# Optimization experiments

Hardware: AMD Instinct MI355X
Metric: run time of the kernel (lower is better)

## Reference

```python
import jax, jax.numpy as jnp
import numpy as np

K_NEIGHBORS = 16
NUM_PATCHES = 32
W_NORMAL = 1.0
W_SURFVAR = 1.0


def _knn_centered(points, k):
    """points: [B, N, 3] -> k nearest neighbors re-centered at each point, [B, N, k, 3].
    Distances are computed on stop_gradient(points) to match torch's .detach()."""
    pd = jax.lax.stop_gradient(points)
    # squared pairwise distances [B, N, N] (sqrt is monotone -> topk order identical)
    d2 = jnp.sum((pd[:, :, None, :] - pd[:, None, :, :]) ** 2, axis=-1)
    _, idx = jax.lax.top_k(-d2, k)  # smallest-k indices, [B, N, k]
    knn = jax.vmap(lambda pts, id_: pts[id_])(points, idx)  # [B, N, k, 3]
    return knn - points[:, :, None, :]


def _eig_props(knn):
    """knn: [B, N, k, 3] -> (normal [B,N,3] = eigvec of smallest eigval, eigvals [B,N,3] ascending)."""
    cov = jnp.einsum('bnki,bnkj->bnij', knn, knn)  # [B, N, 3, 3]
    w, v = jnp.linalg.eigh(cov)  # ascending eigenvalues, matches torch.symeig
    return v[..., :, 0], w


def setup_inputs() -> dict:
    key = jax.random.key(0)
    pointCloud = jax.random.normal(key, (4, 8192, 3), dtype=jnp.float32)
    return {"pointCloud": pointCloud}


def reference(pointCloud):
    B, N, _ = pointCloud.shape
    pp = N // NUM_PATCHES

    # global kNN / normals / surface variance
    knn_g = _knn_centered(pointCloud, K_NEIGHBORS)
    nrm_g, w_g = _eig_props(knn_g)

    # patchwise: each patch is an independent small point cloud -> fold patches into batch
    patch_pts = pointCloud.reshape(B * NUM_PATCHES, pp, 3)
    knn_p = _knn_centered(patch_pts, K_NEIGHBORS)
    nrm_p, w_p = _eig_props(knn_p)
    nrm_p = nrm_p.reshape(B, N, 3)

    # normal loss (abs variant, sign-ambiguity-free)
    loss_n = jnp.mean(jnp.linalg.norm(jnp.abs(nrm_p) - jnp.abs(nrm_g), axis=2)) * W_NORMAL

    # surface variance loss: lambda_min / sum(lambda)
    sv_g = w_g[..., 0] / jnp.sum(w_g, axis=-1)            # [B, N]
    sv_p = (w_p[..., 0] / jnp.sum(w_p, axis=-1)).reshape(B, N)
    loss_sv = jnp.mean((sv_p - sv_g) ** 2) * W_SURFVAR

    return jnp.stack([loss_n, loss_sv])  # [2] (original returns list of two [1] tensors)
```

## Files before the change

### kernel.cpp

```cpp
#include <hip/hip_runtime.h>
#include <math.h>

#define KNN 16
#define NPTS 8192
#define PTCH 256
#define NPATCH 32
#define NBATCH 4
#define NQ 32
#define SSTRIDE 130
#define LAMBDA_T 64.0f

#define NC 16
#define NCELLS (NC * NC * NC)
#define GMIN -4.2f
#define ICS 1.9047619f

__device__ __forceinline__ float lam_f(float r, float s)
{
    const float C     = 0.063493636f;
    const float SQ2PI = 2.5066283f;
    const float IS2   = 0.70710678f;
    float a = fabsf(r - s), b = r + s;
    float amr = a - r;
    float coefA = amr * amr + 2.f - s * s;
    float I = 2.f * __expf(-0.5f * b * b) - coefA * __expf(-0.5f * a * a)
            + r * SQ2PI * (erff(b * IS2) - erff(a * IS2));
    float M = C * (3.14159265f / r) * I;
    if (s > r) {
        float u = s - r;
        M += 12.566371f * C * (1.2533141f * erff(u * IS2) - u * __expf(-0.5f * u * u));
    }
    return (float)NPTS * M;
}

__device__ __forceinline__ void jrot(double& app, double& aqq, double& apq,
                                     double& arp, double& arq,
                                     double& vp0, double& vq0,
                                     double& vp1, double& vq1,
                                     double& vp2, double& vq2)
{
    double g = apq;
    if (g == 0.0) return;
    double theta = (aqq - app) / (2.0 * g);
    double at = fabs(theta);
    double t = (at > 1.0e154) ? (0.5 / theta)
                              : (copysign(1.0, theta) / (at + sqrt(theta * theta + 1.0)));
    double c = 1.0 / sqrt(t * t + 1.0);
    double s = t * c;
    double tau = s / (1.0 + c);
    app -= t * g;
    aqq += t * g;
    apq = 0.0;
    double rp = arp, rq = arq;
    arp = rp - s * (rq + tau * rp);
    arq = rq + s * (rp - tau * rq);
    double p0 = vp0, q0 = vq0;
    vp0 = p0 - s * (q0 + tau * p0); vq0 = q0 + s * (p0 - tau * q0);
    double p1 = vp1, q1 = vq1;
    vp1 = p1 - s * (q1 + tau * p1); vq1 = q1 + s * (p1 - tau * q1);
    double p2 = vp2, q2 = vq2;
    vp2 = p2 - s * (q2 + tau * p2); vq2 = q2 + s * (p2 - tau * q2);
}

__device__ __forceinline__ void eig3(double a00, double a11, double a22,
                                     double a01, double a02, double a12,
                                     double& nx, double& ny, double& nz,
                                     double& lmin, double& lsum)
{
    double v00 = 1, v01 = 0, v02 = 0;
    double v10 = 0, v11 = 1, v12 = 0;
    double v20 = 0, v21 = 0, v22 = 1;
    double scale = fabs(a00) + fabs(a11) + fabs(a22) + fabs(a01) + fabs(a02) + fabs(a12);
    if (scale > 0.0) {
        for (int sweep = 0; sweep < 6; ++sweep) {
            double off = fabs(a01) + fabs(a02) + fabs(a12);
            if (off <= scale * 1e-15) break;
            jrot(a00, a11, a01, a02, a12, v00, v01, v10, v11, v20, v21);
            jrot(a00, a22, a02, a01, a12, v00, v02, v10, v12, v20, v22);
            jrot(a11, a22, a12, a01, a02, v01, v02, v11, v12, v21, v22);
        }
    }
    lsum = a00 + a11 + a22;
    lmin = a00; nx = v00; ny = v10; nz = v20;
    if (a11 < lmin) { lmin = a11; nx = v01; ny = v11; nz = v21; }
    if (a22 < lmin) { lmin = a22; nx = v02; ny = v12; nz = v22; }
}

__device__ __forceinline__ unsigned mkkey(float d2, unsigned idx) {
    return (__float_as_uint(d2) & 0xFFFFE000u) | idx;
}

__device__ __forceinline__ void insert16(unsigned key, unsigned* L)
{
    L[KNN - 1] = key;
    #pragma unroll
    for (int m = KNN - 1; m >= 1; --m) {
        unsigned a = L[m - 1], b = L[m];
        L[m - 1] = min(a, b);
        L[m]     = max(a, b);
    }
}

__device__ __forceinline__ void merge4(unsigned* L, int lane)
{
    #pragma unroll
    for (int step = 1; step <= 2; step <<= 1) {
        unsigned tmp[KNN];
        #pragma unroll
        for (int m = 0; m < KNN; ++m) tmp[m] = __shfl(L[m], lane ^ step, 64);
        for (int m = 0; m < KNN; ++m) {
            if (tmp[m] >= L[KNN - 1]) break;
            insert16(tmp[m], L);
        }
    }
}

__device__ __forceinline__ float rfl(float x) {
    return __int_as_float(__builtin_amdgcn_readfirstlane(__float_as_int(x)));
}
__device__ __forceinline__ unsigned mbcnt64(unsigned long long m) {
    return __builtin_amdgcn_mbcnt_hi((unsigned)(m >> 32),
           __builtin_amdgcn_mbcnt_lo((unsigned)m, 0u));
}

__device__ __forceinline__ int cidx(float v) {
    int i = (int)floorf((v - GMIN) * ICS);
    return min(max(i, 0), NC - 1);
}
__device__ __forceinline__ int cellOf(float x, float y, float z) {
    return (cidx(z) * NC + cidx(y)) * NC + cidx(x);
}

#define BT 1024
__global__ void __launch_bounds__(1024)
build_kernel(const float* __restrict__ pts, float* __restrict__ out,
             unsigned* __restrict__ cellStart, float4* __restrict__ sorted)
{
    __shared__ unsigned hist[NCELLS];
    __shared__ unsigned part[BT];
    const int b = blockIdx.x;
    const int t = threadIdx.x;
    if (b == 0 && t == 0) { out[0] = 0.0f; out[1] = 0.0f; }
    for (int i = t; i < NCELLS; i += BT) hist[i] = 0u;
    __syncthreads();
    const float* base = pts + (size_t)b * (NPTS * 3);
    float px[8], py[8], pz[8];
    int pc[8];
    #pragma unroll
    for (int k = 0; k < 8; ++k) {
        int i = k * BT + t;
        px[k] = base[i * 3 + 0];
        py[k] = base[i * 3 + 1];
        pz[k] = base[i * 3 + 2];
        pc[k] = cellOf(px[k], py[k], pz[k]);
        atomicAdd(&hist[pc[k]], 1u);
    }
    __syncthreads();
    unsigned loc[4], s = 0;
    #pragma unroll
    for (int i = 0; i < 4; ++i) { loc[i] = s; s += hist[t * 4 + i]; }
    part[t] = s;
    __syncthreads();
    for (int o = 1; o < BT; o <<= 1) {
        unsigned u = (t >= o) ? part[t - o] : 0u;
        __syncthreads();
        part[t] += u;
        __syncthreads();
    }
    unsigned basex = part[t] - s;
    unsigned* csb = cellStart + b * (NCELLS + 1);
    #pragma unroll
    for (int i = 0; i < 4; ++i) {
        unsigned e = basex + loc[i];
        csb[t * 4 + i] = e;
        hist[t * 4 + i] = e;
    }
    if (t == BT - 1) csb[NCELLS] = basex + s;
    __syncthreads();
    float4* sb = sorted + (size_t)b * NPTS;
    #pragma unroll
    for (int k = 0; k < 8; ++k) {
        int i = k * BT + t;
        unsigned slot = atomicAdd(&hist[pc[k]], 1u);
        float4 v;
        v.x = px[k]; v.y = py[k]; v.z = pz[k]; v.w = __uint_as_float((unsigned)i);
        sb[slot] = v;
    }
}

__global__ void __launch_bounds__(256)
gate_kernel(const float* __restrict__ pts, float* __restrict__ g2buf)
{
    int q = blockIdx.x * 256 + threadIdx.x;
    int b = q >> 13, i = q & (NPTS - 1);
    const float* pp = pts + (size_t)b * (NPTS * 3) + (size_t)i * 3;
    float x = pp[0], y = pp[1], z = pp[2];
    float r = fmaxf(sqrtf(x * x + y * y + z * z), 0.01f);
    float lo = 0.f, hi = 12.f;
    #pragma unroll 1
    for (int it = 0; it < 16; ++it) {
        float mid = 0.5f * (lo + hi);
        if (lam_f(r, mid) < LAMBDA_T) lo = mid; else hi = mid;
    }
    g2buf[q] = hi * hi;
}

__global__ void __launch_bounds__(256)
filter_kernel(const float* __restrict__ pts, const float* __restrict__ g2buf,
              const unsigned* __restrict__ cellStart,
              const float4* __restrict__ sortedp,
              unsigned* __restrict__ survk, unsigned* __restrict__ cnts)
{
    const int lane = threadIdx.x & 63;
    const int wq = __builtin_amdgcn_readfirstlane(
        (int)((blockIdx.x * 256u + (unsigned)threadIdx.x) >> 6));
    const int b  = wq >> 13;
    const int qi = wq & (NPTS - 1);
    const float* base = pts + (size_t)b * (NPTS * 3);
    const unsigned* cs = cellStart + b * (NCELLS + 1);
    const float4* sp = sortedp + (size_t)b * NPTS;

    const float qx = base[qi * 3 + 0];
    const float qy = base[qi * 3 + 1];
    const float qz = base[qi * 3 + 2];
    const float g2 = g2buf[wq];
    const float g  = sqrtf(g2);

    int ixlo = cidx(qx - g), ixhi = cidx(qx + g);
    int iylo = cidx(qy - g), iyhi = cidx(qy + g);
    int izlo = cidx(qz - g), izhi = cidx(qz + g);
    int nx = ixhi - ixlo + 1;
    int ny = iyhi - iylo + 1;
    int nyz = ny * (izhi - izlo + 1);
    const int lR  = (nyz >= 8) ? 3 : (nyz >= 4) ? 2 : (nyz >= 2) ? 1 : 0;
    const int R   = 1 << lR;
    const int lsl = 6 - lR;
    const unsigned SL = 64u >> lR;
    const unsigned slot = (unsigned)lane & (SL - 1u);
    unsigned cnt = 0;
    unsigned sbase = (unsigned)wq * SSTRIDE;
    #pragma unroll 1
    for (int r0 = 0; r0 < nyz; r0 += 64) {
        int r = r0 + lane;
        unsigned pk = 0;
        if (r < nyz) {
            int iz = izlo + r / ny;
            int iy = iylo + (r - (r / ny) * ny);
            int cb = (iz * NC + iy) * NC + ixlo;
            unsigned sB = cs[cb];
            pk = sB | ((cs[cb + nx] - sB) << 14);
        }
        int rmax = min(nyz - r0, 64);
        int gcount = (rmax + R - 1) >> lR;
        #pragma unroll 1
        for (int gg = 0; gg < gcount; ++gg) {
            unsigned pkm = __shfl(pk, (gg << lR) + (lane >> lsl), 64);
            unsigned sBm = pkm & 0x3FFFu;
            unsigned lm  = pkm >> 14;
            #pragma unroll 1
            for (unsigned st = slot; ; st += SL) {
                bool in = st < lm;
                if (!__any(in ? 1 : 0)) break;
                float4 c = sp[min(sBm + st, (unsigned)(NPTS - 1))];
                float dx = qx - c.x, dy = qy - c.y, dz = qz - c.z;
                float d2 = dx * dx + dy * dy + dz * dz;
                bool pass = in && (d2 < g2);
                unsigned long long m = __ballot(pass);
                if (pass) {
                    unsigned sw = min(cnt + mbcnt64(m), (unsigned)(SSTRIDE - 1));
                    survk[sbase + sw] = mkkey(d2, __float_as_uint(c.w));
                }
                cnt += (unsigned)__popcll(m);
            }
        }
    }
    if (lane == 0) cnts[wq] = cnt;
}

__global__ void __launch_bounds__(256, 4)
select_kernel(const float* __restrict__ pts,
              const float* __restrict__ g2buf,
              const unsigned* __restrict__ survk_g,
              const unsigned* __restrict__ cnts_g,
              double* __restrict__ partials)
{
    __shared__ float4 pbuf4[PTCH];
    __shared__ unsigned survl[NQ * SSTRIDE];
    __shared__ unsigned cnts[NQ];
    __shared__ double xbuf[NQ * 4];
    __shared__ double rb[4];

    const int t = threadIdx.x;
    const int w = t >> 6;
    const int lane = t & 63;
    const int p = blockIdx.x;
    const int eighth = blockIdx.y;
    const int b = blockIdx.z;

    const float* base = pts + (size_t)b * (NPTS * 3);
    const int qbase = p * PTCH + eighth * NQ;
    const int qg0 = b * NPTS + qbase;

    {
        const float* src = base + p * (PTCH * 3);
        float* dst = (float*)pbuf4;
        #pragma unroll
        for (int s = 0; s < 3; ++s) {
            int f = t + s * 256;
            int j = f / 3;
            int c = f - 3 * j;
            dst[j * 4 + c] = src[f];
        }
    }
    {
        const unsigned* src = survk_g + (size_t)qg0 * SSTRIDE;
        #pragma unroll 1
        for (int i = t; i < NQ * SSTRIDE; i += 256) survl[i] = src[i];
        if (t < NQ) cnts[t] = cnts_g[qg0 + t];
    }
    __syncthreads();

    const int qq = lane >> 2;
    const int h = lane & 3;
    const int myq = (w & 1) * 16 + qq;
    float4 qv = pbuf4[eighth * NQ + myq];
    const float pqx = qv.x, pqy = qv.y, pqz = qv.z;

    double ngx = 0, ngy = 0, ngz = 0, svg = 0;

    if (w < 2) {
        unsigned gl[KNN];
        #pragma unroll
        for (int m = 0; m < KNN; ++m) gl[m] = 0xFFFFFFFFu;
        unsigned cnt = cnts[myq];
        bool valid = (cnt >= KNN) && (cnt <= SSTRIDE);
        if (valid) {
            unsigned share = (cnt + 3) >> 2;
            unsigned m0 = h * share;
            unsigned m1 = min(m0 + share, cnt);
            #pragma unroll 4
            for (unsigned m = m0; m < m1; ++m) {
                unsigned k = survl[myq * SSTRIDE + m];
                if (k < gl[KNN - 1]) insert16(k, gl);
            }
        }
        merge4(gl, lane);
        if (valid) {
            float g = g2buf[qg0 + myq];
            float upper = __uint_as_float((gl[KNN - 1] & 0xFFFFE000u) + 0x2000u);
            valid = (upper < g * 0.999f - 1e-5f);
        }
        if (__any((h == 0 && !valid) ? 1 : 0)) {
            if (h == 0 && !valid) {
                #pragma unroll
                for (int m = 0; m < KNN; ++m) gl[m] = 0xFFFFFFFFu;
                #pragma unroll 1
                for (int i = 0; i < NPTS; ++i) {
                    float cx = base[i * 3 + 0];
                    float cy = base[i * 3 + 1];
                    float cz = base[i * 3 + 2];
                    float dx = pqx - cx, dy = pqy - cy, dz = pqz - cz;
                    float d2 = dx * dx + dy * dy + dz * dz;
                    unsigned k = mkkey(d2, (unsigned)i);
                    if (k < gl[KNN - 1]) insert16(k, gl);
                }
            }
        }
        if (h == 0) {
            double c00 = 0, c11 = 0, c22 = 0, c01 = 0, c02 = 0, c12 = 0;
            const double qxd = pqx, qyd = pqy, qzd = pqz;
            #pragma unroll
            for (int m = 0; m < KNN; ++m) {
                int idx = (int)(gl[m] & 0x1FFFu);
                double dx = (double)base[idx * 3 + 0] - qxd;
                double dy = (double)base[idx * 3 + 1] - qyd;
                double dz = (double)base[idx * 3 + 2] - qzd;
                c00 += dx * dx; c11 += dy * dy; c22 += dz * dz;
                c01 += dx * dy; c02 += dx * dz; c12 += dy * dz;
            }
            double lmin, lsum;
            eig3(c00, c11, c22, c01, c02, c12, ngx, ngy, ngz, lmin, lsum);
            svg = lmin / lsum;
        }
    } else {
        unsigned pl[KNN];
        #pragma unroll
        for (int m = 0; m < KNN; ++m) pl[m] = 0xFFFFFFFFu;
        const int j0 = h * 64;
        #pragma unroll 4
        for (int j = j0; j < j0 + 64; ++j) {
            float4 c = pbuf4[j];
            float dx = pqx - c.x, dy = pqy - c.y, dz = pqz - c.z;
            float d2 = dx * dx + dy * dy + dz * dz;
            unsigned k = mkkey(d2, (unsigned)j);
            if (k < pl[KNN - 1]) insert16(k, pl);
        }
        merge4(pl, lane);
        if (h == 0) {
            double c00 = 0, c11 = 0, c22 = 0, c01 = 0, c02 = 0, c12 = 0;
            const double qxd = pqx, qyd = pqy, qzd = pqz;
            #pragma unroll
            for (int m = 0; m < KNN; ++m) {
                int idx = (int)(pl[m] & 0x1FFFu);
                float4 cpt = pbuf4[idx];
                double dx = (double)cpt.x - qxd;
                double dy = (double)cpt.y - qyd;
                double dz = (double)cpt.z - qzd;
                c00 += dx * dx; c11 += dy * dy; c22 += dz * dz;
                c01 += dx * dy; c02 += dx * dz; c12 += dy * dz;
            }
            double nx, ny, nz, lmin, lsum;
            eig3(c00, c11, c22, c01, c02, c12, nx, ny, nz, lmin, lsum);
            xbuf[myq * 4 + 0] = nx;
            xbuf[myq * 4 + 1] = ny;
            xbuf[myq * 4 + 2] = nz;
            xbuf[myq * 4 + 3] = lmin / lsum;
        }
    }
    __syncthreads();

    double ln = 0.0, lsv = 0.0;
    if (w < 2 && h == 0) {
        double npx = xbuf[myq * 4 + 0];
        double npy = xbuf[myq * 4 + 1];
        double npz = xbuf[myq * 4 + 2];
        double svp = xbuf[myq * 4 + 3];
        double dx = fabs(npx) - fabs(ngx);
        double dy = fabs(npy) - fabs(ngy);
        double dz = fabs(npz) - fabs(ngz);
        ln  = sqrt(dx * dx + dy * dy + dz * dz);
        double ds = svp - svg;
        lsv = ds * ds;
    }
    if (w < 2) {
        #pragma unroll
        for (int o = 32; o > 0; o >>= 1) {
            ln  += __shfl_down(ln, o);
            lsv += __shfl_down(lsv, o);
        }
        if (lane == 0) { rb[w * 2 + 0] = ln; rb[w * 2 + 1] = lsv; }
    }
    __syncthreads();
    if (t == 0) {
        const int bf = (b * 8 + eighth) * NPATCH + p;
        partials[bf * 2 + 0] = rb[0] + rb[2];
        partials[bf * 2 + 1] = rb[1] + rb[3];
    }
}

__global__ void __launch_bounds__(256)
reduce_kernel(const double* __restrict__ partials, float* __restrict__ out)
{
    __shared__ double sln[4], slv[4];
    const int t = threadIdx.x;
    double a = 0.0, c = 0.0;
    #pragma unroll
    for (int k = 0; k < 4; ++k) {
        int i = t + k * 256;
        a += partials[i * 2 + 0];
        c += partials[i * 2 + 1];
    }
    #pragma unroll
    for (int o = 32; o > 0; o >>= 1) {
        a += __shfl_down(a, o);
        c += __shfl_down(c, o);
    }
    if ((t & 63) == 0) { sln[t >> 6] = a; slv[t >> 6] = c; }
    __syncthreads();
    if (t == 0) {
        const double inv = 1.0 / (double)(NBATCH * NPTS);
        out[0] = (float)((sln[0] + sln[1] + sln[2] + sln[3]) * inv);
        out[1] = (float)((slv[0] + slv[1] + slv[2] + slv[3]) * inv);
    }
}

__global__ void __launch_bounds__(256, 4)
spl_main(const float* __restrict__ pts, float* __restrict__ out,
         const unsigned* __restrict__ cellStart, const float4* __restrict__ sortedp)
{
    __shared__ float4 pbuf4[PTCH];
    __shared__ unsigned survk[NQ * SSTRIDE];
    __shared__ unsigned cnts[NQ];
    __shared__ float gbuf[NQ];
    __shared__ double xbuf[NQ * 4];
    __shared__ double rb[4];

    const int t = threadIdx.x;
    const int w = t >> 6;
    const int lane = t & 63;
    const int p = blockIdx.x;
    const int eighth = blockIdx.y;
    const int b = blockIdx.z;

    const float* base = pts + (size_t)b * (NPTS * 3);
    const int qbase = p * PTCH + eighth * NQ;
    const unsigned* cs = cellStart + b * (NCELLS + 1);
    const float4* sp = sortedp + (size_t)b * NPTS;

    {
        const float* src = base + p * (PTCH * 3);
        float* dst = (float*)pbuf4;
        #pragma unroll
        for (int s = 0; s < 3; ++s) {
            int f = t + s * 256;
            int j = f / 3;
            int c = f - 3 * j;
            dst[j * 4 + c] = src[f];
        }
    }
    if (t < NQ) {
        int qi = qbase + t;
        float x = base[qi * 3 + 0], y = base[qi * 3 + 1], z = base[qi * 3 + 2];
        float r = fmaxf(sqrtf(x * x + y * y + z * z), 0.01f);
        float lo = 0.f, hi = 12.f;
        #pragma unroll 1
        for (int it = 0; it < 16; ++it) {
            float mid = 0.5f * (lo + hi);
            if (lam_f(r, mid) < LAMBDA_T) lo = mid; else hi = mid;
        }
        gbuf[t] = hi * hi;
    }
    __syncthreads();

    #pragma unroll 1
    for (int u = 0; u < 8; ++u) {
        const int q = w * 8 + u;
        float4 qv = pbuf4[eighth * NQ + q];
        float qx = rfl(qv.x), qy = rfl(qv.y), qz = rfl(qv.z);
        float g2 = rfl(gbuf[q]);
        float g = sqrtf(g2);
        int ixlo = cidx(qx - g), ixhi = cidx(qx + g);
        int iylo = cidx(qy - g), iyhi = cidx(qy + g);
        int izlo = cidx(qz - g), izhi = cidx(qz + g);
        int nx = ixhi - ixlo + 1;
        int ny = iyhi - iylo + 1;
        int nyz = ny * (izhi - izlo + 1);
        const int lR  = (nyz >= 8) ? 3 : (nyz >= 4) ? 2 : (nyz >= 2) ? 1 : 0;
        const int R   = 1 << lR;
        const int lsl = 6 - lR;
        const unsigned SL = 64u >> lR;
        const unsigned slot = (unsigned)lane & (SL - 1u);
        unsigned cnt = 0;
        unsigned sbase = (unsigned)q * SSTRIDE;
        #pragma unroll 1
        for (int r0 = 0; r0 < nyz; r0 += 64) {
            int r = r0 + lane;
            unsigned pk = 0;
            if (r < nyz) {
                int iz = izlo + r / ny;
                int iy = iylo + (r - (r / ny) * ny);
                int cb = (iz * NC + iy) * NC + ixlo;
                unsigned sB = cs[cb];
                pk = sB | ((cs[cb + nx] - sB) << 14);
            }
            int rmax = min(nyz - r0, 64);
            int gcount = (rmax + R - 1) >> lR;
            #pragma unroll 1
            for (int gg = 0; gg < gcount; ++gg) {
                unsigned pkm = __shfl(pk, (gg << lR) + (lane >> lsl), 64);
                unsigned sBm = pkm & 0x3FFFu;
                unsigned lm  = pkm >> 14;
                #pragma unroll 1
                for (unsigned st = slot; ; st += SL) {
                    bool in = st < lm;
                    if (!__any(in ? 1 : 0)) break;
                    float4 c = sp[min(sBm + st, (unsigned)(NPTS - 1))];
                    float dx = qx - c.x, dy = qy - c.y, dz = qz - c.z;
                    float d2 = dx * dx + dy * dy + dz * dz;
                    bool pass = in && (d2 < g2);
                    unsigned long long m = __ballot(pass);
                    if (pass) {
                        unsigned sw = min(cnt + mbcnt64(m), (unsigned)(SSTRIDE - 1));
                        survk[sbase + sw] = mkkey(d2, __float_as_uint(c.w));
                    }
                    cnt += (unsigned)__popcll(m);
                }
            }
        }
        if (lane == 0) cnts[q] = cnt;
    }
    __syncthreads();

    const int qq = lane >> 2;
    const int h = lane & 3;
    const int myq = (w & 1) * 16 + qq;
    float4 qv = pbuf4[eighth * NQ + myq];
    const float pqx = qv.x, pqy = qv.y, pqz = qv.z;

    double ngx = 0, ngy = 0, ngz = 0, svg = 0;

    if (w < 2) {
        unsigned gl[KNN];
        #pragma unroll
        for (int m = 0; m < KNN; ++m) gl[m] = 0xFFFFFFFFu;
        unsigned cnt = cnts[myq];
        bool valid = (cnt >= KNN) && (cnt <= SSTRIDE);
        if (valid) {
            unsigned share = (cnt + 3) >> 2;
            unsigned m0 = h * share;
            unsigned m1 = min(m0 + share, cnt);
            #pragma unroll 1
            for (unsigned m = m0; m < m1; ++m) {
                unsigned k = survk[myq * SSTRIDE + m];
                if (k < gl[KNN - 1]) insert16(k, gl);
            }
        }
        merge4(gl, lane);
        if (valid) {
            float g = gbuf[myq];
            float upper = __uint_as_float((gl[KNN - 1] & 0xFFFFE000u) + 0x2000u);
            valid = (upper < g * 0.999f - 1e-5f);
        }
        if (__any((h == 0 && !valid) ? 1 : 0)) {
            if (h == 0 && !valid) {
                #pragma unroll
                for (int m = 0; m < KNN; ++m) gl[m] = 0xFFFFFFFFu;
                #pragma unroll 1
                for (int i = 0; i < NPTS; ++i) {
                    float cx = base[i * 3 + 0];
                    float cy = base[i * 3 + 1];
                    float cz = base[i * 3 + 2];
                    float dx = pqx - cx, dy = pqy - cy, dz = pqz - cz;
                    float d2 = dx * dx + dy * dy + dz * dz;
                    unsigned k = mkkey(d2, (unsigned)i);
                    if (k < gl[KNN - 1]) insert16(k, gl);
                }
            }
        }
        if (h == 0) {
            double c00 = 0, c11 = 0, c22 = 0, c01 = 0, c02 = 0, c12 = 0;
            const double qxd = pqx, qyd = pqy, qzd = pqz;
            #pragma unroll
            for (int m = 0; m < KNN; ++m) {
                int idx = (int)(gl[m] & 0x1FFFu);
                double dx = (double)base[idx * 3 + 0] - qxd;
                double dy = (double)base[idx * 3 + 1] - qyd;
                double dz = (double)base[idx * 3 + 2] - qzd;
                c00 += dx * dx; c11 += dy * dy; c22 += dz * dz;
                c01 += dx * dy; c02 += dx * dz; c12 += dy * dz;
            }
            double lmin, lsum;
            eig3(c00, c11, c22, c01, c02, c12, ngx, ngy, ngz, lmin, lsum);
            svg = lmin / lsum;
        }
    } else {
        unsigned pl[KNN];
        #pragma unroll
        for (int m = 0; m < KNN; ++m) pl[m] = 0xFFFFFFFFu;
        const int j0 = h * 64;
        #pragma unroll 1
        for (int j = j0; j < j0 + 64; ++j) {
            float4 c = pbuf4[j];
            float dx = pqx - c.x, dy = pqy - c.y, dz = pqz - c.z;
            float d2 = dx * dx + dy * dy + dz * dz;
            unsigned k = mkkey(d2, (unsigned)j);
            if (k < pl[KNN - 1]) insert16(k, pl);
        }
        merge4(pl, lane);
        if (h == 0) {
            double c00 = 0, c11 = 0, c22 = 0, c01 = 0, c02 = 0, c12 = 0;
            const double qxd = pqx, qyd = pqy, qzd = pqz;
            #pragma unroll
            for (int m = 0; m < KNN; ++m) {
                int idx = (int)(pl[m] & 0x1FFFu);
                float4 cpt = pbuf4[idx];
                double dx = (double)cpt.x - qxd;
                double dy = (double)cpt.y - qyd;
                double dz = (double)cpt.z - qzd;
                c00 += dx * dx; c11 += dy * dy; c22 += dz * dz;
                c01 += dx * dy; c02 += dx * dz; c12 += dy * dz;
            }
            double nx, ny, nz, lmin, lsum;
            eig3(c00, c11, c22, c01, c02, c12, nx, ny, nz, lmin, lsum);
            xbuf[myq * 4 + 0] = nx;
            xbuf[myq * 4 + 1] = ny;
            xbuf[myq * 4 + 2] = nz;
            xbuf[myq * 4 + 3] = lmin / lsum;
        }
    }
    __syncthreads();

    double ln = 0.0, lsv = 0.0;
    if (w < 2 && h == 0) {
        double npx = xbuf[myq * 4 + 0];
        double npy = xbuf[myq * 4 + 1];
        double npz = xbuf[myq * 4 + 2];
        double svp = xbuf[myq * 4 + 3];
        double dx = fabs(npx) - fabs(ngx);
        double dy = fabs(npy) - fabs(ngy);
        double dz = fabs(npz) - fabs(ngz);
        ln  = sqrt(dx * dx + dy * dy + dz * dz);
        double ds = svp - svg;
        lsv = ds * ds;
    }
    if (w < 2) {
        #pragma unroll
        for (int o = 32; o > 0; o >>= 1) {
            ln  += __shfl_down(ln, o);
            lsv += __shfl_down(lsv, o);
        }
        if (lane == 0) { rb[w * 2 + 0] = ln; rb[w * 2 + 1] = lsv; }
    }
    __syncthreads();
    if (t == 0) {
        const double inv = 1.0 / (double)(NBATCH * NPTS);
        atomicAdd(&out[0], (float)((rb[0] + rb[2]) * inv));
        atomicAdd(&out[1], (float)((rb[1] + rb[3]) * inv));
    }
}

extern "C" void kernel_launch(void* const* d_in, const int* in_sizes, int n_in,
                              void* d_out, int out_size, void* d_ws, size_t ws_size,
                              hipStream_t stream)
{
    const float* pts = (const float*)d_in[0];
    float* out = (float*)d_out;

    unsigned char* ws = (unsigned char*)d_ws;
    unsigned* cellStart = (unsigned*)(ws);
    float4*   sorted    = (float4*)  (ws + 65552);
    float*    g2buf     = (float*)   (ws + 589840);
    unsigned* cnts      = (unsigned*)(ws + 720912);
    unsigned* survk     = (unsigned*)(ws + 851984);
    double*   partials  = (double*)  (ws + 17891344);

    hipLaunchKernelGGL(build_kernel, dim3(NBATCH), dim3(BT), 0, stream,
                       pts, out, cellStart, sorted);
    if (ws_size >= (size_t)17907728) {
        hipLaunchKernelGGL(gate_kernel, dim3(NBATCH * NPTS / 256), dim3(256), 0, stream,
                           pts, g2buf);
        hipLaunchKernelGGL(filter_kernel, dim3(NBATCH * NPTS / 4), dim3(256), 0, stream,
                           pts, g2buf, cellStart, sorted, survk, cnts);
        dim3 grid(NPATCH, 8, NBATCH);
        hipLaunchKernelGGL(select_kernel, grid, dim3(256), 0, stream,
                           pts, g2buf, survk, cnts, partials);
        hipLaunchKernelGGL(reduce_kernel, dim3(1), dim3(256), 0, stream,
                           partials, out);
    } else {
        dim3 grid(NPATCH, 8, NBATCH);
        hipLaunchKernelGGL(spl_main, grid, dim3(256), 0, stream,
                           pts, out, cellStart, sorted);
    }
}
```

Baseline: 160.9 us.

## Split covariance/eigen work out of select kernel into dedicated eig_loss kernel

The select kernel now only finds global and patch kNN indices and writes them to a workspace buffer. A new kernel uses one thread per (query, global/patch) pair to build the covariance, run the double-precision 3x3 eigen solve, and compute the loss terms, pairing the two results with a lane shuffle. Previously only one lane in four per query did the eigen work while the other lanes idled, so this spreads that work across all threads. The cost is an extra kernel launch and an index buffer round-trip through global memory, and the workspace size threshold for the fast path rises.

```diff
diff --git a/kernel.cpp b/kernel.cpp
--- a/kernel.cpp
+++ b/kernel.cpp
@@ -282,13 +282,11 @@
               const float* __restrict__ g2buf,
               const unsigned* __restrict__ survk_g,
               const unsigned* __restrict__ cnts_g,
-              double* __restrict__ partials)
+              unsigned* __restrict__ idx16)
 {
     __shared__ float4 pbuf4[PTCH];
     __shared__ unsigned survl[NQ * SSTRIDE];
     __shared__ unsigned cnts[NQ];
-    __shared__ double xbuf[NQ * 4];
-    __shared__ double rb[4];
 
     const int t = threadIdx.x;
     const int w = t >> 6;
@@ -325,8 +323,6 @@
     const int myq = (w & 1) * 16 + qq;
     float4 qv = pbuf4[eighth * NQ + myq];
     const float pqx = qv.x, pqy = qv.y, pqz = qv.z;
-
-    double ngx = 0, ngy = 0, ngz = 0, svg = 0;
 
     if (w < 2) {
         unsigned gl[KNN];
@@ -367,20 +363,9 @@
             }
         }
         if (h == 0) {
-            double c00 = 0, c11 = 0, c22 = 0, c01 = 0, c02 = 0, c12 = 0;
-            const double qxd = pqx, qyd = pqy, qzd = pqz;
+            unsigned* dst = idx16 + (size_t)(qg0 + myq) * 32;
             #pragma unroll
-            for (int m = 0; m < KNN; ++m) {
-                int idx = (int)(gl[m] & 0x1FFFu);
-                double dx = (double)base[idx * 3 + 0] - qxd;
-                double dy = (double)base[idx * 3 + 1] - qyd;
-                double dz = (double)base[idx * 3 + 2] - qzd;
-                c00 += dx * dx; c11 += dy * dy; c22 += dz * dz;
-                c01 += dx * dy; c02 += dx * dz; c12 += dy * dz;
-            }
-            double lmin, lsum;
-            eig3(c00, c11, c22, c01, c02, c12, ngx, ngy, ngz, lmin, lsum);
-            svg = lmin / lsum;
+            for (int m = 0; m < KNN; ++m) dst[m] = gl[m] & 0x1FFFu;
         }
     } else {
         unsigned pl[KNN];
@@ -397,54 +382,71 @@
         }
         merge4(pl, lane);
         if (h == 0) {
-            double c00 = 0, c11 = 0, c22 = 0, c01 = 0, c02 = 0, c12 = 0;
-            const double qxd = pqx, qyd = pqy, qzd = pqz;
+            unsigned* dst = idx16 + (size_t)(qg0 + myq) * 32 + 16;
             #pragma unroll
-            for (int m = 0; m < KNN; ++m) {
-                int idx = (int)(pl[m] & 0x1FFFu);
-                float4 cpt = pbuf4[idx];
-                double dx = (double)cpt.x - qxd;
-                double dy = (double)cpt.y - qyd;
-                double dz = (double)cpt.z - qzd;
-                c00 += dx * dx; c11 += dy * dy; c22 += dz * dz;
-                c01 += dx * dy; c02 += dx * dz; c12 += dy * dz;
-            }
-            double nx, ny, nz, lmin, lsum;
-            eig3(c00, c11, c22, c01, c02, c12, nx, ny, nz, lmin, lsum);
-            xbuf[myq * 4 + 0] = nx;
-            xbuf[myq * 4 + 1] = ny;
-            xbuf[myq * 4 + 2] = nz;
-            xbuf[myq * 4 + 3] = lmin / lsum;
-        }
-    }
-    __syncthreads();
+            for (int m = 0; m < KNN; ++m)
+                dst[m] = (unsigned)(p * PTCH) + (pl[m] & 0x1FFFu);
+        }
+    }
+}
+
+__global__ void __launch_bounds__(256)
+eig_loss_kernel(const float* __restrict__ pts,
+                const unsigned* __restrict__ idx16,
+                double* __restrict__ partials)
+{
+    __shared__ double sln[4], slv[4];
+    const int t = threadIdx.x;
+    const int e = blockIdx.x * 256 + t;
+    const int qid = e >> 1;
+    const int b = qid >> 13;
+    const int qi = qid & (NPTS - 1);
+    const float* base = pts + (size_t)b * (NPTS * 3);
+
+    const double qxd = (double)base[qi * 3 + 0];
+    const double qyd = (double)base[qi * 3 + 1];
+    const double qzd = (double)base[qi * 3 + 2];
+
+    const unsigned* L = idx16 + (size_t)qid * 32 + (e & 1) * 16;
+    double c00 = 0, c11 = 0, c22 = 0, c01 = 0, c02 = 0, c12 = 0;
+    #pragma unroll
+    for (int m = 0; m < KNN; ++m) {
+        int idx = (int)L[m];
+        double dx = (double)base[idx * 3 + 0] - qxd;
+        double dy = (double)base[idx * 3 + 1] - qyd;
+        double dz = (double)base[idx * 3 + 2] - qzd;
+        c00 += dx * dx; c11 += dy * dy; c22 += dz * dz;
+        c01 += dx * dy; c02 += dx * dz; c12 += dy * dz;
+    }
+    double nx, ny, nz, lmin, lsum;
+    eig3(c00, c11, c22, c01, c02, c12, nx, ny, nz, lmin, lsum);
+    double sv = lmin / lsum;
+
+    double onx = __shfl_xor(nx, 1, 64);
+    double ony = __shfl_xor(ny, 1, 64);
+    double onz = __shfl_xor(nz, 1, 64);
+    double osv = __shfl_xor(sv, 1, 64);
 
     double ln = 0.0, lsv = 0.0;
-    if (w < 2 && h == 0) {
-        double npx = xbuf[myq * 4 + 0];
-        double npy = xbuf[myq * 4 + 1];
-        double npz = xbuf[myq * 4 + 2];
-        double svp = xbuf[myq * 4 + 3];
-        double dx = fabs(npx) - fabs(ngx);
-        double dy = fabs(npy) - fabs(ngy);
-        double dz = fabs(npz) - fabs(ngz);
+    if ((e & 1) == 0) {
+        double dx = fabs(onx) - fabs(nx);
+        double dy = fabs(ony) - fabs(ny);
+        double dz = fabs(onz) - fabs(nz);
         ln  = sqrt(dx * dx + dy * dy + dz * dz);
-        double ds = svp - svg;
+        double ds = osv - sv;
         lsv = ds * ds;
     }
-    if (w < 2) {
-        #pragma unroll
-        for (int o = 32; o > 0; o >>= 1) {
-            ln  += __shfl_down(ln, o);
-            lsv += __shfl_down(lsv, o);
-        }
-        if (lane == 0) { rb[w * 2 + 0] = ln; rb[w * 2 + 1] = lsv; }
-    }
+    #pragma unroll
+    for (int o = 32; o > 0; o >>= 1) {
+        ln  += __shfl_down(ln, o);
+        lsv += __shfl_down(lsv, o);
+    }
+    const int w = t >> 6;
+    if ((t & 63) == 0) { sln[w] = ln; slv[w] = lsv; }
     __syncthreads();
     if (t == 0) {
-        const int bf = (b * 8 + eighth) * NPATCH + p;
-        partials[bf * 2 + 0] = rb[0] + rb[2];
-        partials[bf * 2 + 1] = rb[1] + rb[3];
+        partials[blockIdx.x * 2 + 0] = sln[0] + sln[1] + sln[2] + sln[3];
+        partials[blockIdx.x * 2 + 1] = slv[0] + slv[1] + slv[2] + slv[3];
     }
 }
 
@@ -453,13 +455,8 @@
 {
     __shared__ double sln[4], slv[4];
     const int t = threadIdx.x;
-    double a = 0.0, c = 0.0;
-    #pragma unroll
-    for (int k = 0; k < 4; ++k) {
-        int i = t + k * 256;
-        a += partials[i * 2 + 0];
-        c += partials[i * 2 + 1];
-    }
+    double a = partials[t * 2 + 0];
+    double c = partials[t * 2 + 1];
     #pragma unroll
     for (int o = 32; o > 0; o >>= 1) {
         a += __shfl_down(a, o);
@@ -722,18 +719,21 @@
     float*    g2buf     = (float*)   (ws + 589840);
     unsigned* cnts      = (unsigned*)(ws + 720912);
     unsigned* survk     = (unsigned*)(ws + 851984);
-    double*   partials  = (double*)  (ws + 17891344);
+    unsigned* idx16     = (unsigned*)(ws + 17891344);
+    double*   partials  = (double*)  (ws + 22085648);
 
     hipLaunchKernelGGL(build_kernel, dim3(NBATCH), dim3(BT), 0, stream,
                        pts, out, cellStart, sorted);
-    if (ws_size >= (size_t)17907728) {
+    if (ws_size >= (size_t)22089744) {
         hipLaunchKernelGGL(gate_kernel, dim3(NBATCH * NPTS / 256), dim3(256), 0, stream,
                            pts, g2buf);
         hipLaunchKernelGGL(filter_kernel, dim3(NBATCH * NPTS / 4), dim3(256), 0, stream,
                            pts, g2buf, cellStart, sorted, survk, cnts);
         dim3 grid(NPATCH, 8, NBATCH);
         hipLaunchKernelGGL(select_kernel, grid, dim3(256), 0, stream,
-                           pts, g2buf, survk, cnts, partials);
+                           pts, g2buf, survk, cnts, idx16);
+        hipLaunchKernelGGL(eig_loss_kernel, dim3(NBATCH * NPTS * 2 / 256), dim3(256),
+                           0, stream, pts, idx16, partials);
         hipLaunchKernelGGL(reduce_kernel, dim3(1), dim3(256), 0, stream,
                            partials, out);
     } else {
```

Result: faster. 157.0 us (-2.4%).
